# Kernel optimization log

Hardware: AMD Instinct MI355X
Metric: run time of the kernel (lower is better)

## Reference

```python
import jax, jax.numpy as jnp
import numpy as np

N = 50000      # nodes
E = 800000     # edges
IN = 64        # in_channels
HID = 256      # hidden_dim
LAT = 64       # latent_dim
KS = 2         # kernel_size per dim
DIM = 3        # pseudo-coordinate dim
K = KS ** DIM  # 8 spline weight matrices


def spline_basis_coeffs(pseudo, ks, dim, dtype):
    """Degree-1 open B-spline basis: returns per-edge coefficients c [E, ks**dim]."""
    e = pseudo.shape[0]
    v = pseudo * (ks - 1)                                   # [E, dim]
    bot = jnp.clip(jnp.floor(v), 0, ks - 1).astype(jnp.int32)
    frac = v - bot
    c = jnp.zeros((e, ks ** dim), dtype)
    rows = jnp.arange(e)
    for s in range(2 ** dim):  # 8 knot combinations (fixed small loop)
        w = jnp.ones(e, dtype)
        idx = jnp.zeros(e, jnp.int32)
        for d in range(dim):
            bit = (s >> d) & 1
            w = w * (frac[:, d] if bit else 1.0 - frac[:, d])
            idx = idx + jnp.clip(bot[:, d] + bit, 0, ks - 1) * (ks ** d)
        c = c.at[rows, idx].add(w)
    return c


def spline_conv(x, edge_index, pseudo, W, Wroot, b):
    """SplineConv with aggr='mean', root weight and bias (degree-1 open splines)."""
    src, dst = edge_index[0], edge_index[1]
    n = x.shape[0]
    e = pseudo.shape[0]
    c = spline_basis_coeffs(pseudo, KS, DIM, x.dtype)        # [E, K]
    x_src = x[src]                                           # [E, in] gather
    deg = jax.ops.segment_sum(jnp.ones(e, x.dtype), dst, num_segments=n)
    inv_deg = (1.0 / jnp.maximum(deg, 1.0))[:, None]         # [N, 1] mean aggr
    out = jnp.zeros((n, W.shape[2]), x.dtype)
    for k in range(W.shape[0]):  # K=8 fixed loop; scatter-add then dense matmul
        agg = jax.ops.segment_sum(c[:, k:k + 1] * x_src, dst, num_segments=n)
        out = out + (agg * inv_deg) @ W[k]
    return out + x @ Wroot + b


def setup_inputs() -> dict:
    key = jax.random.key(0)
    ks = jax.random.split(key, 12)
    x = jax.random.normal(ks[0], (N, IN), jnp.float32)
    edge_index = jax.random.randint(ks[1], (2, E), 0, N, jnp.int32)
    s = 0.05
    return {
        "x": x,
        "edge_index": edge_index,
        "conv1_W": jax.random.normal(ks[2], (K, IN, HID), jnp.float32) * s,
        "conv1_root": jax.random.normal(ks[3], (IN, HID), jnp.float32) * s,
        "conv1_b": jnp.zeros((HID,), jnp.float32),
        "conv2_W": jax.random.normal(ks[4], (K, HID, LAT), jnp.float32) * s,
        "conv2_root": jax.random.normal(ks[5], (HID, LAT), jnp.float32) * s,
        "conv2_b": jnp.zeros((LAT,), jnp.float32),
        "dec_w1": jax.random.normal(ks[6], (LAT, HID), jnp.float32) * s,
        "dec_b1": jnp.zeros((HID,), jnp.float32),
        "dec_w2": jax.random.normal(ks[7], (HID, IN), jnp.float32) * s,
        "dec_b2": jnp.zeros((IN,), jnp.float32),
    }


def reference(x, edge_index, conv1_W, conv1_root, conv1_b,
              conv2_W, conv2_root, conv2_b,
              dec_w1, dec_b1, dec_w2, dec_b2):
    pseudo = jnp.zeros((edge_index.shape[1], DIM), x.dtype)  # forward builds zeros
    h = jax.nn.relu(spline_conv(x, edge_index, pseudo, conv1_W, conv1_root, conv1_b))
    z = spline_conv(h, edge_index, pseudo, conv2_W, conv2_root, conv2_b)
    h2 = jax.nn.relu(z @ dec_w1 + dec_b1)
    return h2 @ dec_w2 + dec_b2
```

## Files before the change

### kernel.cpp

```cpp
#include <hip/hip_runtime.h>
#include <hip/hip_bf16.h>


#define THREADS 256

typedef __attribute__((ext_vector_type(8))) short bf16x8;
typedef __attribute__((ext_vector_type(4))) float f32x4;

__device__ __forceinline__ float bf2f(unsigned short u) {
    unsigned v = ((unsigned)u) << 16;
    return __builtin_bit_cast(float, v);
}
__device__ __forceinline__ unsigned short f2bf(float f) {
    __hip_bfloat16 h = __float2bfloat16(f);
    return __builtin_bit_cast(unsigned short, h);
}

__device__ __forceinline__ void pack_one(unsigned short* dst,
                                         const float* W0, const float* W1,
                                         int NB, int ksplit, int colsplit,
                                         int ld0, int ld1, int t) {
    int i = t & 7, lane = (t >> 3) & 63, rest = t >> 9;
    int j = rest % NB, s = rest / NB;
    int k = s * 32 + ((lane >> 4) << 3) + i;
    int c = (j << 4) + (lane & 15);
    float v;
    if (c >= colsplit)    v = W1[(size_t)k * ld1 + (c - colsplit)];
    else if (k >= ksplit) v = W1[(size_t)(k - ksplit) * ld1 + c];
    else                  v = W0[(size_t)k * ld0 + c];
    dst[t] = f2bf(v);
}

#define BIG (1 << 30)

__global__ void prep_kernel(const float* __restrict__ W1g, const float* __restrict__ root1,
                            const float* __restrict__ W2g, const float* __restrict__ root2,
                            const float* __restrict__ dw1, const float* __restrict__ dw2,
                            const float* __restrict__ x, const int* __restrict__ dstv,
                            int* __restrict__ bcnt,
                            unsigned short* __restrict__ Pb1,
                            unsigned short* __restrict__ Pb2,
                            unsigned short* __restrict__ Pd1,
                            unsigned short* __restrict__ Pd2,
                            unsigned short* __restrict__ ab1,
                            int n, int E, int pb_pack) {
    if ((int)blockIdx.x >= pb_pack) {
        __shared__ int hist[256];
        int t = threadIdx.x;
        hist[t] = 0;
        __syncthreads();
        int e0 = ((int)blockIdx.x - pb_pack) * 4096;
#pragma unroll
        for (int i = 0; i < 16; ++i) {
            int e = e0 + t + i * 256;
            if (e < E) atomicAdd(&hist[dstv[e] >> 8], 1);
        }
        __syncthreads();
        int h = hist[t];
        if (h) atomicAdd(&bcnt[t], h);
        return;
    }
    int t = blockIdx.x * blockDim.x + threadIdx.x;
    if (t < 32768) {
        pack_one(Pb1, W1g, root1, 16, 64, BIG, 256, 256, t);
    } else if (t < 65536) {
        pack_one(Pb2, W2g, root2, 8, BIG, 64, 64, 64, t - 32768);
    } else if (t < 81920) {
        pack_one(Pd1, dw1, dw1, 16, BIG, BIG, 256, 256, t - 65536);
    } else if (t < 98304) {
        pack_one(Pd2, dw2, dw2, 4, BIG, BIG, 64, 64, t - 81920);
    } else if (t < 98304 + n * 64) {
        int u = t - 98304;
        int row = u >> 6, col = u & 63;
        ab1[(size_t)row * 128 + 64 + col] = f2bf(x[(size_t)row * 64 + col]);
    }
}

__global__ void scan_buckets(const int* __restrict__ bcnt, int* __restrict__ bbase,
                             int* __restrict__ bcur, int* __restrict__ offs,
                             int nbkt, int N, int E) {
    __shared__ int sm[256];
    int t = threadIdx.x;
    int v = (t < nbkt) ? bcnt[t] : 0;
    sm[t] = v;
    __syncthreads();
    for (int off = 1; off < 256; off <<= 1) {
        int xv = (t >= off) ? sm[t - off] : 0;
        __syncthreads();
        sm[t] += xv;
        __syncthreads();
    }
    int ex = sm[t] - v;
    bbase[t] = ex;
    bcur[t] = ex;
    if (t == 0) { bbase[256] = E; offs[N] = E; }
}

__global__ __launch_bounds__(256) void partition_edges(
    const int* __restrict__ src, const int* __restrict__ dst,
    int* __restrict__ bcur, int* __restrict__ epack, int E) {
    __shared__ int hist[256];
    __shared__ int base[256];
    __shared__ int lcur[256];
    int t = threadIdx.x;
    hist[t] = 0;
    __syncthreads();
    int e0 = blockIdx.x * 4096;
    int myd[16], mys[16];
#pragma unroll
    for (int i = 0; i < 16; ++i) {
        int e = e0 + t + i * 256;
        int d = (e < E) ? dst[e] : -1;
        mys[i] = (e < E) ? src[e] : 0;
        myd[i] = d;
        if (d >= 0) atomicAdd(&hist[d >> 8], 1);
    }
    __syncthreads();
    int h = hist[t];
    if (h > 0) base[t] = atomicAdd(&bcur[t], h);
    lcur[t] = 0;
    __syncthreads();
#pragma unroll
    for (int i = 0; i < 16; ++i) {
        int d = myd[i];
        if (d >= 0) {
            int b = d >> 8;
            int p = atomicAdd(&lcur[b], 1);
            epack[base[b] + p] = ((d & 255) << 20) | mys[i];
        }
    }
}

__global__ __launch_bounds__(256) void bucket_fill2(
    const int* __restrict__ epack, const int* __restrict__ bbase,
    int* __restrict__ offs, float* __restrict__ invd,
    int* __restrict__ esrc, int N) {
    __shared__ int nh[256];
    __shared__ int loff[256];
    __shared__ int ncur[256];
    __shared__ int stage[8192];
    int b = blockIdx.x, t = threadIdx.x;
    int n0 = b << 8;
    int cntn = min(256, N - n0);
    int ebase = bbase[b];
    int ecount = bbase[b + 1] - ebase;
    nh[t] = 0;
    __syncthreads();
    for (int i = t; i < ecount; i += 256)
        atomicAdd(&nh[epack[ebase + i] >> 20], 1);
    __syncthreads();
    int v = nh[t];
    loff[t] = v;
    __syncthreads();
    for (int off = 1; off < 256; off <<= 1) {
        int xv = (t >= off) ? loff[t - off] : 0;
        __syncthreads();
        loff[t] += xv;
        __syncthreads();
    }
    int ex = loff[t] - v;
    loff[t] = ex;
    if (t < cntn) {
        offs[n0 + t] = ebase + ex;
        invd[n0 + t] = 1.0f / (float)max(v, 1);
    }
    ncur[t] = 0;
    __syncthreads();
    bool useLds = (ecount <= 8192);
    for (int i = t; i < ecount; i += 256) {
        int p = epack[ebase + i];
        int dl = p >> 20;
        int pos = atomicAdd(&ncur[dl], 1);
        int g = loff[dl] + pos;
        int sv = p & 0xFFFFF;
        if (useLds) stage[g] = sv;
        else        esrc[ebase + g] = sv;
    }
    __syncthreads();
    if (useLds)
        for (int i = t; i < ecount; i += 256) esrc[ebase + i] = stage[i];
}

__global__ void agg_x_pair(unsigned short* __restrict__ ab1, const int* __restrict__ esrc,
                           const int* __restrict__ offs, const float* __restrict__ invd,
                           int n) {
    int node = blockIdx.x * 4 + (threadIdx.x >> 6);
    if (node >= n) return;
    int l = threadIdx.x & 63;
    int slot = l >> 5, c = l & 31;
    const unsigned short* xb = ab1 + 64 + c * 2;
    int s = offs[node], e = offs[node + 1];
    float a0 = 0.f, a1 = 0.f, b0 = 0.f, b1 = 0.f;
    float c0 = 0.f, c1 = 0.f, d0 = 0.f, d1 = 0.f;
    int j = s;
    for (; j + 8 <= e; j += 8) {
        int i0 = esrc[j + slot], i1 = esrc[j + 2 + slot];
        int i2 = esrc[j + 4 + slot], i3 = esrc[j + 6 + slot];
        unsigned v0 = *(const unsigned*)(xb + (size_t)i0 * 128);
        unsigned v1 = *(const unsigned*)(xb + (size_t)i1 * 128);
        unsigned v2 = *(const unsigned*)(xb + (size_t)i2 * 128);
        unsigned v3 = *(const unsigned*)(xb + (size_t)i3 * 128);
        a0 += bf2f((unsigned short)v0); a1 += bf2f((unsigned short)(v0 >> 16));
        b0 += bf2f((unsigned short)v1); b1 += bf2f((unsigned short)(v1 >> 16));
        c0 += bf2f((unsigned short)v2); c1 += bf2f((unsigned short)(v2 >> 16));
        d0 += bf2f((unsigned short)v3); d1 += bf2f((unsigned short)(v3 >> 16));
    }
    for (; j + 2 <= e; j += 2) {
        int i0 = esrc[j + slot];
        unsigned v0 = *(const unsigned*)(xb + (size_t)i0 * 128);
        a0 += bf2f((unsigned short)v0); a1 += bf2f((unsigned short)(v0 >> 16));
    }
    if (j < e && slot == 0) {
        int i0 = esrc[j];
        unsigned v0 = *(const unsigned*)(xb + (size_t)i0 * 128);
        a0 += bf2f((unsigned short)v0); a1 += bf2f((unsigned short)(v0 >> 16));
    }
    float r0 = (a0 + b0) + (c0 + d0), r1 = (a1 + b1) + (c1 + d1);
    r0 += __shfl_xor(r0, 32);
    r1 += __shfl_xor(r1, 32);
    if (slot == 0) {
        float iv = invd[node];
        unsigned o = ((unsigned)f2bf(r1 * iv) << 16) | (unsigned)f2bf(r0 * iv);
        *(unsigned*)(ab1 + (size_t)node * 128 + c * 2) = o;
    }
}

__global__ void agg_z_pair(const unsigned short* __restrict__ hwroot,
                           const int* __restrict__ esrc, const int* __restrict__ offs,
                           const float* __restrict__ invd, const float* __restrict__ b2,
                           unsigned short* __restrict__ z, int n) {
    int node = blockIdx.x * 4 + (threadIdx.x >> 6);
    if (node >= n) return;
    int l = threadIdx.x & 63;
    int slot = l >> 5, c = l & 31;
    const unsigned short* hb = hwroot + c * 2;
    int s = offs[node], e = offs[node + 1];
    float a0 = 0.f, a1 = 0.f, b0 = 0.f, b1 = 0.f;
    float c0 = 0.f, c1 = 0.f, d0 = 0.f, d1 = 0.f;
    int j = s;
    for (; j + 8 <= e; j += 8) {
        int i0 = esrc[j + slot], i1 = esrc[j + 2 + slot];
        int i2 = esrc[j + 4 + slot], i3 = esrc[j + 6 + slot];
        unsigned v0 = *(const unsigned*)(hb + (size_t)i0 * 128);
        unsigned v1 = *(const unsigned*)(hb + (size_t)i1 * 128);
        unsigned v2 = *(const unsigned*)(hb + (size_t)i2 * 128);
        unsigned v3 = *(const unsigned*)(hb + (size_t)i3 * 128);
        a0 += bf2f((unsigned short)v0); a1 += bf2f((unsigned short)(v0 >> 16));
        b0 += bf2f((unsigned short)v1); b1 += bf2f((unsigned short)(v1 >> 16));
        c0 += bf2f((unsigned short)v2); c1 += bf2f((unsigned short)(v2 >> 16));
        d0 += bf2f((unsigned short)v3); d1 += bf2f((unsigned short)(v3 >> 16));
    }
    for (; j + 2 <= e; j += 2) {
        int i0 = esrc[j + slot];
        unsigned v0 = *(const unsigned*)(hb + (size_t)i0 * 128);
        a0 += bf2f((unsigned short)v0); a1 += bf2f((unsigned short)(v0 >> 16));
    }
    if (j < e && slot == 0) {
        int i0 = esrc[j];
        unsigned v0 = *(const unsigned*)(hb + (size_t)i0 * 128);
        a0 += bf2f((unsigned short)v0); a1 += bf2f((unsigned short)(v0 >> 16));
    }
    float r0 = (a0 + b0) + (c0 + d0), r1 = (a1 + b1) + (c1 + d1);
    r0 += __shfl_xor(r0, 32);
    r1 += __shfl_xor(r1, 32);
    if (slot == 0) {
        float iv = invd[node];
        unsigned hr = *(const unsigned*)(hwroot + (size_t)node * 128 + 64 + c * 2);
        float v0 = r0 * iv + bf2f((unsigned short)hr) + b2[c * 2];
        float v1 = r1 * iv + bf2f((unsigned short)(hr >> 16)) + b2[c * 2 + 1];
        unsigned o = ((unsigned)f2bf(v1) << 16) | (unsigned)f2bf(v0);
        *(unsigned*)(z + (size_t)node * 64 + c * 2) = o;
    }
}

template <int K1, int NBW2, bool OUTBF>
__global__ __launch_bounds__(256) void gemm_fused(
    const unsigned short* __restrict__ A,
    const unsigned short* __restrict__ Bp1, const float* __restrict__ bias1,
    const unsigned short* __restrict__ Bp2, const float* __restrict__ bias2,
    void* __restrict__ Cv, int n)
{
    constexpr int KS1 = K1 / 32;
    constexpr int N2 = NBW2 * 64;
    constexpr int NB2 = NBW2 * 4;
    __shared__ unsigned short ht[64][264];

    const int m0 = blockIdx.x * 64;
    const int lane = threadIdx.x & 63;
    const int w = threadIdx.x >> 6;
    const int quad = lane >> 4;
    const int l16 = lane & 15;

    {
        f32x4 acc[4][4] = {};
        const unsigned short* Arow = A + (size_t)(m0 + l16) * K1 + quad * 8;
        for (int s = 0; s < KS1; ++s) {
            bf16x8 a[4];
#pragma unroll
            for (int mb = 0; mb < 4; ++mb)
                a[mb] = *(const bf16x8*)(Arow + (size_t)mb * 16 * K1 + s * 32);
#pragma unroll
            for (int jn = 0; jn < 4; ++jn) {
                int j = w * 4 + jn;
                bf16x8 b = *(const bf16x8*)(Bp1 + ((size_t)(s * 16 + j) * 64 + lane) * 8);
#pragma unroll
                for (int mb = 0; mb < 4; ++mb)
                    acc[mb][jn] = __builtin_amdgcn_mfma_f32_16x16x32_bf16(a[mb], b, acc[mb][jn], 0, 0, 0);
            }
        }
#pragma unroll
        for (int jn = 0; jn < 4; ++jn) {
            int col = (w * 4 + jn) * 16 + l16;
            float bv = bias1[col];
#pragma unroll
            for (int mb = 0; mb < 4; ++mb)
#pragma unroll
                for (int r = 0; r < 4; ++r) {
                    int row = mb * 16 + quad * 4 + r;
                    ht[row][col] = f2bf(fmaxf(acc[mb][jn][r] + bv, 0.f));
                }
        }
    }
    __syncthreads();

    {
        f32x4 acc[4][NBW2] = {};
        for (int s = 0; s < 8; ++s) {
            bf16x8 a[4];
#pragma unroll
            for (int mb = 0; mb < 4; ++mb)
                a[mb] = *(const bf16x8*)&ht[mb * 16 + l16][s * 32 + quad * 8];
#pragma unroll
            for (int jn = 0; jn < NBW2; ++jn) {
                int j = w * NBW2 + jn;
                bf16x8 b = *(const bf16x8*)(Bp2 + ((size_t)(s * NB2 + j) * 64 + lane) * 8);
#pragma unroll
                for (int mb = 0; mb < 4; ++mb)
                    acc[mb][jn] = __builtin_amdgcn_mfma_f32_16x16x32_bf16(a[mb], b, acc[mb][jn], 0, 0, 0);
            }
        }
#pragma unroll
        for (int jn = 0; jn < NBW2; ++jn) {
            int col = (w * NBW2 + jn) * 16 + l16;
            float bv = bias2 ? bias2[col] : 0.f;
#pragma unroll
            for (int mb = 0; mb < 4; ++mb)
#pragma unroll
                for (int r = 0; r < 4; ++r) {
                    int row = m0 + mb * 16 + quad * 4 + r;
                    if (row < n) {
                        float v = acc[mb][jn][r] + bv;
                        if (OUTBF)
                            ((unsigned short*)Cv)[(size_t)row * N2 + col] = f2bf(v);
                        else
                            ((float*)Cv)[(size_t)row * N2 + col] = v;
                    }
                }
        }
    }
}

extern "C" void kernel_launch(void* const* d_in, const int* in_sizes, int n_in,
                              void* d_out, int out_size, void* d_ws, size_t ws_size,
                              hipStream_t stream) {
    const float* x      = (const float*)d_in[0];
    const int*   ei     = (const int*)d_in[1];
    const float* W1g    = (const float*)d_in[2];
    const float* root1  = (const float*)d_in[3];
    const float* b1     = (const float*)d_in[4];
    const float* W2g    = (const float*)d_in[5];
    const float* root2  = (const float*)d_in[6];
    const float* b2     = (const float*)d_in[7];
    const float* dw1    = (const float*)d_in[8];
    const float* db1    = (const float*)d_in[9];
    const float* dw2    = (const float*)d_in[10];
    const float* db2    = (const float*)d_in[11];
    float* out = (float*)d_out;

    const int N = in_sizes[0] / 64;
    const int E = in_sizes[1] / 2;
    const int Npad = N + 64;
    const int* srcv = ei;
    const int* dstv = ei + E;

    char* ws = (char*)d_ws;
    auto alloc = [&](size_t bytes) -> void* {
        void* p = (void*)ws;
        ws += (bytes + 255) & ~(size_t)255;
        return p;
    };
    int*   bcnt   = (int*)alloc(1024);
    int*   bbase  = (int*)alloc(1056);
    int*   bcur   = (int*)alloc(1024);
    int*   offs   = (int*)alloc((size_t)(N + 1) * 4);
    float* invd   = (float*)alloc((size_t)N * 4);
    int*   esrc   = (int*)alloc((size_t)E * 4);
    int*   epack  = (int*)alloc((size_t)E * 4);
    unsigned short* Pb1 = (unsigned short*)alloc(32768 * 2);
    unsigned short* Pb2 = (unsigned short*)alloc(32768 * 2);
    unsigned short* Pd1 = (unsigned short*)alloc(16384 * 2);
    unsigned short* Pd2 = (unsigned short*)alloc(16384 * 2);
    unsigned short* ab1    = (unsigned short*)alloc((size_t)Npad * 128 * 2);
    unsigned short* hwroot = (unsigned short*)alloc((size_t)Npad * 128 * 2);
    unsigned short* z      = (unsigned short*)alloc((size_t)Npad * 64 * 2);

    hipMemsetAsync(bcnt, 0, 1024, stream);

    int gb = (N + 63) / 64;
    int nbkt = (N + 255) / 256;
    int pa = (E + 4095) / 4096;
    int pb_pack = (98304 + N * 64 + THREADS - 1) / THREADS;

    prep_kernel<<<pb_pack + pa, THREADS, 0, stream>>>(
        W1g, root1, W2g, root2, dw1, dw2, x, dstv, bcnt,
        Pb1, Pb2, Pd1, Pd2, ab1, N, E, pb_pack);
    scan_buckets<<<1, 256, 0, stream>>>(bcnt, bbase, bcur, offs, nbkt, N, E);
    partition_edges<<<pa, 256, 0, stream>>>(srcv, dstv, bcur, epack, E);
    bucket_fill2<<<nbkt, 256, 0, stream>>>(epack, bbase, offs, invd, esrc, N);

    agg_x_pair<<<(N + 3) / 4, THREADS, 0, stream>>>(ab1, esrc, offs, invd, N);
    gemm_fused<128, 2, true><<<gb, 256, 0, stream>>>(ab1, Pb1, b1, Pb2, nullptr, hwroot, N);
    agg_z_pair<<<(N + 3) / 4, THREADS, 0, stream>>>(hwroot, esrc, offs, invd, b2, z, N);
    gemm_fused<64, 1, false><<<gb, 256, 0, stream>>>(z, Pd1, db1, Pd2, db2, out, N);
}
```

Measured before the change: 212.9 us.

## Fold bucket scan into partition/fill kernels and widen gathers to 4 channels

Removes the single-block scan_buckets launch: partition_edges and bucket_fill2 each recompute the bucket prefix sum from bcnt in shared memory, and bcur now holds relative offsets starting from zero via the enlarged memset. The aggregation kernels switch from 2-channel 32-bit gathers to 4-channel 64-bit gathers with 4 edge slots per wavefront, and the x-to-bf16 conversion uses float4 loads. This cuts one launch and doubles bytes per gather request, at the cost of redundant per-block scans and more shuffles.

```diff
diff --git a/kernel.cpp b/kernel.cpp
--- a/kernel.cpp
+++ b/kernel.cpp
@@ -14,6 +14,12 @@
 __device__ __forceinline__ unsigned short f2bf(float f) {
     __hip_bfloat16 h = __float2bfloat16(f);
     return __builtin_bit_cast(unsigned short, h);
+}
+__device__ __forceinline__ void acc4(float* f, uint2 v) {
+    f[0] += bf2f((unsigned short)v.x);
+    f[1] += bf2f((unsigned short)(v.x >> 16));
+    f[2] += bf2f((unsigned short)v.y);
+    f[3] += bf2f((unsigned short)(v.y >> 16));
 }
 
 __device__ __forceinline__ void pack_one(unsigned short* dst,
@@ -69,39 +75,25 @@
         pack_one(Pd1, dw1, dw1, 16, BIG, BIG, 256, 256, t - 65536);
     } else if (t < 98304) {
         pack_one(Pd2, dw2, dw2, 4, BIG, BIG, 64, 64, t - 81920);
-    } else if (t < 98304 + n * 64) {
+    } else if (t < 98304 + n * 16) {
         int u = t - 98304;
-        int row = u >> 6, col = u & 63;
-        ab1[(size_t)row * 128 + 64 + col] = f2bf(x[(size_t)row * 64 + col]);
-    }
-}
-
-__global__ void scan_buckets(const int* __restrict__ bcnt, int* __restrict__ bbase,
-                             int* __restrict__ bcur, int* __restrict__ offs,
-                             int nbkt, int N, int E) {
-    __shared__ int sm[256];
-    int t = threadIdx.x;
-    int v = (t < nbkt) ? bcnt[t] : 0;
-    sm[t] = v;
-    __syncthreads();
-    for (int off = 1; off < 256; off <<= 1) {
-        int xv = (t >= off) ? sm[t - off] : 0;
-        __syncthreads();
-        sm[t] += xv;
-        __syncthreads();
-    }
-    int ex = sm[t] - v;
-    bbase[t] = ex;
-    bcur[t] = ex;
-    if (t == 0) { bbase[256] = E; offs[N] = E; }
+        int row = u >> 4, c4 = (u & 15) * 4;
+        float4 v = *(const float4*)(x + (size_t)row * 64 + c4);
+        unsigned lo = (unsigned)f2bf(v.x) | ((unsigned)f2bf(v.y) << 16);
+        unsigned hi = (unsigned)f2bf(v.z) | ((unsigned)f2bf(v.w) << 16);
+        uint2 o; o.x = lo; o.y = hi;
+        *(uint2*)(ab1 + (size_t)row * 128 + 64 + c4) = o;
+    }
 }
 
 __global__ __launch_bounds__(256) void partition_edges(
     const int* __restrict__ src, const int* __restrict__ dst,
-    int* __restrict__ bcur, int* __restrict__ epack, int E) {
+    const int* __restrict__ bcnt, int* __restrict__ bcur,
+    int* __restrict__ epack, int E) {
     __shared__ int hist[256];
     __shared__ int base[256];
     __shared__ int lcur[256];
+    __shared__ int bb[256];
     int t = threadIdx.x;
     hist[t] = 0;
     __syncthreads();
@@ -115,9 +107,18 @@
         myd[i] = d;
         if (d >= 0) atomicAdd(&hist[d >> 8], 1);
     }
-    __syncthreads();
+    int cb = bcnt[t];
+    bb[t] = cb;
+    __syncthreads();
+    for (int off = 1; off < 256; off <<= 1) {
+        int xv = (t >= off) ? bb[t - off] : 0;
+        __syncthreads();
+        bb[t] += xv;
+        __syncthreads();
+    }
+    int bbase_t = bb[t] - cb;
     int h = hist[t];
-    if (h > 0) base[t] = atomicAdd(&bcur[t], h);
+    if (h > 0) base[t] = bbase_t + atomicAdd(&bcur[t], h);
     lcur[t] = 0;
     __syncthreads();
 #pragma unroll
@@ -132,9 +133,10 @@
 }
 
 __global__ __launch_bounds__(256) void bucket_fill2(
-    const int* __restrict__ epack, const int* __restrict__ bbase,
+    const int* __restrict__ epack, const int* __restrict__ bcnt,
     int* __restrict__ offs, float* __restrict__ invd,
     int* __restrict__ esrc, int N) {
+    __shared__ int sb_[256];
     __shared__ int nh[256];
     __shared__ int loff[256];
     __shared__ int ncur[256];
@@ -142,8 +144,18 @@
     int b = blockIdx.x, t = threadIdx.x;
     int n0 = b << 8;
     int cntn = min(256, N - n0);
-    int ebase = bbase[b];
-    int ecount = bbase[b + 1] - ebase;
+    int cb = bcnt[t];
+    sb_[t] = cb;
+    __syncthreads();
+    for (int off = 1; off < 256; off <<= 1) {
+        int xv = (t >= off) ? sb_[t - off] : 0;
+        __syncthreads();
+        sb_[t] += xv;
+        __syncthreads();
+    }
+    int ebase = b ? sb_[b - 1] : 0;
+    int ecount = sb_[b] - ebase;
+    if (b == 0 && t == 0) offs[N] = sb_[255];
     nh[t] = 0;
     __syncthreads();
     for (int i = t; i < ecount; i += 256)
@@ -181,95 +193,103 @@
         for (int i = t; i < ecount; i += 256) esrc[ebase + i] = stage[i];
 }
 
-__global__ void agg_x_pair(unsigned short* __restrict__ ab1, const int* __restrict__ esrc,
-                           const int* __restrict__ offs, const float* __restrict__ invd,
-                           int n) {
+__global__ void agg_x4(unsigned short* __restrict__ ab1, const int* __restrict__ esrc,
+                       const int* __restrict__ offs, const float* __restrict__ invd,
+                       int n) {
     int node = blockIdx.x * 4 + (threadIdx.x >> 6);
     if (node >= n) return;
     int l = threadIdx.x & 63;
-    int slot = l >> 5, c = l & 31;
-    const unsigned short* xb = ab1 + 64 + c * 2;
+    int slot = l >> 4, c = l & 15;
+    const unsigned short* xb = ab1 + 64 + c * 4;
     int s = offs[node], e = offs[node + 1];
-    float a0 = 0.f, a1 = 0.f, b0 = 0.f, b1 = 0.f;
-    float c0 = 0.f, c1 = 0.f, d0 = 0.f, d1 = 0.f;
+    float a0[4] = {}, a1[4] = {}, a2[4] = {}, a3[4] = {};
     int j = s;
-    for (; j + 8 <= e; j += 8) {
-        int i0 = esrc[j + slot], i1 = esrc[j + 2 + slot];
-        int i2 = esrc[j + 4 + slot], i3 = esrc[j + 6 + slot];
-        unsigned v0 = *(const unsigned*)(xb + (size_t)i0 * 128);
-        unsigned v1 = *(const unsigned*)(xb + (size_t)i1 * 128);
-        unsigned v2 = *(const unsigned*)(xb + (size_t)i2 * 128);
-        unsigned v3 = *(const unsigned*)(xb + (size_t)i3 * 128);
-        a0 += bf2f((unsigned short)v0); a1 += bf2f((unsigned short)(v0 >> 16));
-        b0 += bf2f((unsigned short)v1); b1 += bf2f((unsigned short)(v1 >> 16));
-        c0 += bf2f((unsigned short)v2); c1 += bf2f((unsigned short)(v2 >> 16));
-        d0 += bf2f((unsigned short)v3); d1 += bf2f((unsigned short)(v3 >> 16));
-    }
-    for (; j + 2 <= e; j += 2) {
+    for (; j + 16 <= e; j += 16) {
+        int i0 = esrc[j + slot],      i1 = esrc[j + 4 + slot];
+        int i2 = esrc[j + 8 + slot],  i3 = esrc[j + 12 + slot];
+        uint2 v0 = *(const uint2*)(xb + (size_t)i0 * 128);
+        uint2 v1 = *(const uint2*)(xb + (size_t)i1 * 128);
+        uint2 v2 = *(const uint2*)(xb + (size_t)i2 * 128);
+        uint2 v3 = *(const uint2*)(xb + (size_t)i3 * 128);
+        acc4(a0, v0); acc4(a1, v1); acc4(a2, v2); acc4(a3, v3);
+    }
+    for (; j + 4 <= e; j += 4) {
         int i0 = esrc[j + slot];
-        unsigned v0 = *(const unsigned*)(xb + (size_t)i0 * 128);
-        a0 += bf2f((unsigned short)v0); a1 += bf2f((unsigned short)(v0 >> 16));
-    }
-    if (j < e && slot == 0) {
-        int i0 = esrc[j];
-        unsigned v0 = *(const unsigned*)(xb + (size_t)i0 * 128);
-        a0 += bf2f((unsigned short)v0); a1 += bf2f((unsigned short)(v0 >> 16));
-    }
-    float r0 = (a0 + b0) + (c0 + d0), r1 = (a1 + b1) + (c1 + d1);
-    r0 += __shfl_xor(r0, 32);
-    r1 += __shfl_xor(r1, 32);
+        uint2 v0 = *(const uint2*)(xb + (size_t)i0 * 128);
+        acc4(a0, v0);
+    }
+    int rem = e - j;
+    if (slot < rem) {
+        int i0 = esrc[j + slot];
+        uint2 v0 = *(const uint2*)(xb + (size_t)i0 * 128);
+        acc4(a1, v0);
+    }
+    float r[4];
+#pragma unroll
+    for (int k = 0; k < 4; ++k) {
+        r[k] = (a0[k] + a1[k]) + (a2[k] + a3[k]);
+        r[k] += __shfl_xor(r[k], 16);
+        r[k] += __shfl_xor(r[k], 32);
+    }
     if (slot == 0) {
         float iv = invd[node];
-        unsigned o = ((unsigned)f2bf(r1 * iv) << 16) | (unsigned)f2bf(r0 * iv);
-        *(unsigned*)(ab1 + (size_t)node * 128 + c * 2) = o;
-    }
-}
-
-__global__ void agg_z_pair(const unsigned short* __restrict__ hwroot,
-                           const int* __restrict__ esrc, const int* __restrict__ offs,
-                           const float* __restrict__ invd, const float* __restrict__ b2,
-                           unsigned short* __restrict__ z, int n) {
+        unsigned lo = (unsigned)f2bf(r[0] * iv) | ((unsigned)f2bf(r[1] * iv) << 16);
+        unsigned hi = (unsigned)f2bf(r[2] * iv) | ((unsigned)f2bf(r[3] * iv) << 16);
+        uint2 o; o.x = lo; o.y = hi;
+        *(uint2*)(ab1 + (size_t)node * 128 + c * 4) = o;
+    }
+}
+
+__global__ void agg_z4(const unsigned short* __restrict__ hwroot,
+                       const int* __restrict__ esrc, const int* __restrict__ offs,
+                       const float* __restrict__ invd, const float* __restrict__ b2,
+                       unsigned short* __restrict__ z, int n) {
     int node = blockIdx.x * 4 + (threadIdx.x >> 6);
     if (node >= n) return;
     int l = threadIdx.x & 63;
-    int slot = l >> 5, c = l & 31;
-    const unsigned short* hb = hwroot + c * 2;
+    int slot = l >> 4, c = l & 15;
+    const unsigned short* hb = hwroot + c * 4;
     int s = offs[node], e = offs[node + 1];
-    float a0 = 0.f, a1 = 0.f, b0 = 0.f, b1 = 0.f;
-    float c0 = 0.f, c1 = 0.f, d0 = 0.f, d1 = 0.f;
+    float a0[4] = {}, a1[4] = {}, a2[4] = {}, a3[4] = {};
     int j = s;
-    for (; j + 8 <= e; j += 8) {
-        int i0 = esrc[j + slot], i1 = esrc[j + 2 + slot];
-        int i2 = esrc[j + 4 + slot], i3 = esrc[j + 6 + slot];
-        unsigned v0 = *(const unsigned*)(hb + (size_t)i0 * 128);
-        unsigned v1 = *(const unsigned*)(hb + (size_t)i1 * 128);
-        unsigned v2 = *(const unsigned*)(hb + (size_t)i2 * 128);
-        unsigned v3 = *(const unsigned*)(hb + (size_t)i3 * 128);
-        a0 += bf2f((unsigned short)v0); a1 += bf2f((unsigned short)(v0 >> 16));
-        b0 += bf2f((unsigned short)v1); b1 += bf2f((unsigned short)(v1 >> 16));
-        c0 += bf2f((unsigned short)v2); c1 += bf2f((unsigned short)(v2 >> 16));
-        d0 += bf2f((unsigned short)v3); d1 += bf2f((unsigned short)(v3 >> 16));
-    }
-    for (; j + 2 <= e; j += 2) {
+    for (; j + 16 <= e; j += 16) {
+        int i0 = esrc[j + slot],      i1 = esrc[j + 4 + slot];
+        int i2 = esrc[j + 8 + slot],  i3 = esrc[j + 12 + slot];
+        uint2 v0 = *(const uint2*)(hb + (size_t)i0 * 128);
+        uint2 v1 = *(const uint2*)(hb + (size_t)i1 * 128);
+        uint2 v2 = *(const uint2*)(hb + (size_t)i2 * 128);
+        uint2 v3 = *(const uint2*)(hb + (size_t)i3 * 128);
+        acc4(a0, v0); acc4(a1, v1); acc4(a2, v2); acc4(a3, v3);
+    }
+    for (; j + 4 <= e; j += 4) {
         int i0 = esrc[j + slot];
-        unsigned v0 = *(const unsigned*)(hb + (size_t)i0 * 128);
-        a0 += bf2f((unsigned short)v0); a1 += bf2f((unsigned short)(v0 >> 16));
-    }
-    if (j < e && slot == 0) {
-        int i0 = esrc[j];
-        unsigned v0 = *(const unsigned*)(hb + (size_t)i0 * 128);
-        a0 += bf2f((unsigned short)v0); a1 += bf2f((unsigned short)(v0 >> 16));
-    }
-    float r0 = (a0 + b0) + (c0 + d0), r1 = (a1 + b1) + (c1 + d1);
-    r0 += __shfl_xor(r0, 32);
-    r1 += __shfl_xor(r1, 32);
+        uint2 v0 = *(const uint2*)(hb + (size_t)i0 * 128);
+        acc4(a0, v0);
+    }
+    int rem = e - j;
+    if (slot < rem) {
+        int i0 = esrc[j + slot];
+        uint2 v0 = *(const uint2*)(hb + (size_t)i0 * 128);
+        acc4(a1, v0);
+    }
+    float r[4];
+#pragma unroll
+    for (int k = 0; k < 4; ++k) {
+        r[k] = (a0[k] + a1[k]) + (a2[k] + a3[k]);
+        r[k] += __shfl_xor(r[k], 16);
+        r[k] += __shfl_xor(r[k], 32);
+    }
     if (slot == 0) {
         float iv = invd[node];
-        unsigned hr = *(const unsigned*)(hwroot + (size_t)node * 128 + 64 + c * 2);
-        float v0 = r0 * iv + bf2f((unsigned short)hr) + b2[c * 2];
-        float v1 = r1 * iv + bf2f((unsigned short)(hr >> 16)) + b2[c * 2 + 1];
-        unsigned o = ((unsigned)f2bf(v1) << 16) | (unsigned)f2bf(v0);
-        *(unsigned*)(z + (size_t)node * 64 + c * 2) = o;
+        uint2 hr = *(const uint2*)(hwroot + (size_t)node * 128 + 64 + c * 4);
+        float v0 = r[0] * iv + bf2f((unsigned short)hr.x) + b2[c * 4 + 0];
+        float v1 = r[1] * iv + bf2f((unsigned short)(hr.x >> 16)) + b2[c * 4 + 1];
+        float v2 = r[2] * iv + bf2f((unsigned short)hr.y) + b2[c * 4 + 2];
+        float v3 = r[3] * iv + bf2f((unsigned short)(hr.y >> 16)) + b2[c * 4 + 3];
+        unsigned lo = (unsigned)f2bf(v0) | ((unsigned)f2bf(v1) << 16);
+        unsigned hi = (unsigned)f2bf(v2) | ((unsigned)f2bf(v3) << 16);
+        uint2 o; o.x = lo; o.y = hi;
+        *(uint2*)(z + (size_t)node * 64 + c * 4) = o;
     }
 }
 
@@ -390,7 +410,6 @@
         return p;
     };
     int*   bcnt   = (int*)alloc(1024);
-    int*   bbase  = (int*)alloc(1056);
     int*   bcur   = (int*)alloc(1024);
     int*   offs   = (int*)alloc((size_t)(N + 1) * 4);
     float* invd   = (float*)alloc((size_t)N * 4);
@@ -404,22 +423,21 @@
     unsigned short* hwroot = (unsigned short*)alloc((size_t)Npad * 128 * 2);
     unsigned short* z      = (unsigned short*)alloc((size_t)Npad * 64 * 2);
 
-    hipMemsetAsync(bcnt, 0, 1024, stream);
+    hipMemsetAsync(bcnt, 0, 2048, stream);
 
     int gb = (N + 63) / 64;
     int nbkt = (N + 255) / 256;
     int pa = (E + 4095) / 4096;
-    int pb_pack = (98304 + N * 64 + THREADS - 1) / THREADS;
+    int pb_pack = (98304 + N * 16 + THREADS - 1) / THREADS;
 
     prep_kernel<<<pb_pack + pa, THREADS, 0, stream>>>(
         W1g, root1, W2g, root2, dw1, dw2, x, dstv, bcnt,
         Pb1, Pb2, Pd1, Pd2, ab1, N, E, pb_pack);
-    scan_buckets<<<1, 256, 0, stream>>>(bcnt, bbase, bcur, offs, nbkt, N, E);
-    partition_edges<<<pa, 256, 0, stream>>>(srcv, dstv, bcur, epack, E);
-    bucket_fill2<<<nbkt, 256, 0, stream>>>(epack, bbase, offs, invd, esrc, N);
-
-    agg_x_pair<<<(N + 3) / 4, THREADS, 0, stream>>>(ab1, esrc, offs, invd, N);
+    partition_edges<<<pa, 256, 0, stream>>>(srcv, dstv, bcnt, bcur, epack, E);
+    bucket_fill2<<<nbkt, 256, 0, stream>>>(epack, bcnt, offs, invd, esrc, N);
+
+    agg_x4<<<(N + 3) / 4, THREADS, 0, stream>>>(ab1, esrc, offs, invd, N);
     gemm_fused<128, 2, true><<<gb, 256, 0, stream>>>(ab1, Pb1, b1, Pb2, nullptr, hwroot, N);
-    agg_z_pair<<<(N + 3) / 4, THREADS, 0, stream>>>(hwroot, esrc, offs, invd, b2, z, N);
+    agg_z4<<<(N + 3) / 4, THREADS, 0, stream>>>(hwroot, esrc, offs, invd, b2, z, N);
     gemm_fused<64, 1, false><<<gb, 256, 0, stream>>>(z, Pd1, db1, Pd2, db2, out, N);
 }
```

Result: faster. 208.6 us (-2.0%).
